# Performance work log

Measured on AMD Instinct MI355X. Metric: run time of the kernel, lower is better.

Reference implementation:

```python
import jax, jax.numpy as jnp
import numpy as np

D_MODEL = 1024
NUM_HEADS = 16
D_HEAD = D_MODEL // NUM_HEADS


def setup_inputs() -> dict:
    key = jax.random.key(0)
    ks = jax.random.split(key, 7)
    B, S = 2, 2048
    scale = 1.0 / np.sqrt(D_MODEL)
    return {
        "x": jax.random.normal(ks[0], (B, S, D_MODEL), dtype=jnp.float32),
        "attn_weights": jnp.zeros((1,), dtype=jnp.float32),  # unused in original forward
        "Wq": jax.random.normal(ks[1], (D_MODEL, D_MODEL), dtype=jnp.float32) * scale,
        "Wk": jax.random.normal(ks[2], (D_MODEL, D_MODEL), dtype=jnp.float32) * scale,
        "Wv": jax.random.normal(ks[3], (D_MODEL, D_MODEL), dtype=jnp.float32) * scale,
        "Wp": jax.random.normal(ks[4], (D_MODEL, D_MODEL), dtype=jnp.float32) * scale,
        "bp": jnp.zeros((D_MODEL,), dtype=jnp.float32),
    }


def reference(x, attn_weights, Wq, Wk, Wv, Wp, bp):
    B, S, D = x.shape
    H, Dh = NUM_HEADS, D_HEAD
    # torch Linear: y = x @ W.T  (weights stored [out, in])
    q = (x @ Wq.T).reshape(B, S, H, Dh).transpose(0, 2, 1, 3)  # [B,H,S,Dh]
    k = (x @ Wk.T).reshape(B, S, H, Dh).transpose(0, 2, 1, 3)
    v = (x @ Wv.T).reshape(B, S, H, Dh).transpose(0, 2, 1, 3)
    # NOTE: original module applies NO 1/sqrt(d) scaling
    scores = jnp.einsum("bhqd,bhkd->bhqk", q, k)
    weights = jax.nn.softmax(scores, axis=-1)  # dropout is inference no-op
    out = jnp.einsum("bhqk,bhkd->bhqd", weights, v)
    out = out.transpose(0, 2, 1, 3).reshape(B, S, D)
    return out @ Wp.T + bp
```

## Files before the change

### kernel.cpp

```cpp
#include <hip/hip_runtime.h>
#include <hip/hip_bf16.h>

#define D_MODEL 1024
#define NUM_HEADS 16
#define D_HEAD 64
#define BATCH 2
#define SEQ 2048
#define TOKENS (BATCH * SEQ)

typedef __attribute__((ext_vector_type(8))) short bf16x8;
typedef __attribute__((ext_vector_type(4))) float f32x4;
typedef __attribute__((ext_vector_type(2))) unsigned int uint2v;

typedef __attribute__((address_space(1))) const unsigned int as1_uint;
typedef __attribute__((address_space(3))) unsigned int as3_uint;

#define LOG2E 1.44269504088896340736f

static __device__ __forceinline__ unsigned short f2bf(float f) {
    unsigned int u = __builtin_bit_cast(unsigned int, f);
    u += 0x7fffu + ((u >> 16) & 1u);
    return (unsigned short)(u >> 16);
}

static __device__ __forceinline__ unsigned int pk2bf(float a, float b) {
    __hip_bfloat162 h = __float22bfloat162_rn(float2{a, b});
    unsigned int u;
    __builtin_memcpy(&u, &h, 4);
    return u;
}

static __device__ __forceinline__ float fast_exp2(float x) {
    return __builtin_amdgcn_exp2f(x);
}

__global__ __launch_bounds__(256) void convert_bf16(
    const float* __restrict__ x,  const float* __restrict__ Wq,
    const float* __restrict__ Wk, const float* __restrict__ Wv,
    const float* __restrict__ Wp,
    unsigned short* __restrict__ xb,  unsigned short* __restrict__ Wqb,
    unsigned short* __restrict__ Wkb, unsigned short* __restrict__ Wvb,
    unsigned short* __restrict__ Wpb)
{
    int v = blockIdx.x * 256 + threadIdx.x;
    const float* s;
    unsigned short* d;
    int off;
    if (v < (1 << 20)) { s = x; d = xb; off = v; }
    else {
        int u = v - (1 << 20);
        int w = u >> 18;
        off = u & ((1 << 18) - 1);
        s = (w == 0) ? Wq : (w == 1) ? Wk : (w == 2) ? Wv : Wp;
        d = (w == 0) ? Wqb : (w == 1) ? Wkb : (w == 2) ? Wvb : Wpb;
    }
    float4 f = ((const float4*)s)[off];
    ushort4 o = { f2bf(f.x), f2bf(f.y), f2bf(f.z), f2bf(f.w) };
    ((ushort4*)d)[off] = o;
}

__global__ __launch_bounds__(512, 4) void qkv_gemm(
    const unsigned short* __restrict__ xb,
    const unsigned short* __restrict__ Wqb, const unsigned short* __restrict__ Wkb,
    const unsigned short* __restrict__ Wvb,
    unsigned short* __restrict__ Q, unsigned short* __restrict__ Kb,
    unsigned short* __restrict__ Vt)
{
    const int m0 = blockIdx.x * 128;
    const int n0 = blockIdx.y * 64;

    __shared__ __attribute__((aligned(16))) unsigned short sm[40960];

    const int t = threadIdx.x;
    const int wave = t >> 6, lane = t & 63;
    const int wm = (wave & 1) * 64, wn = (wave >> 1) * 16;
    const int l15 = lane & 15, quad = lane >> 4;
    const int sw = l15 & 7;

    const unsigned short* Wz[3] = { Wqb, Wkb, Wvb };

    f32x4 acc[3][4];
#pragma unroll
    for (int z = 0; z < 3; z++)
#pragma unroll
        for (int i = 0; i < 4; i++) acc[z][i] = (f32x4)0.f;

    auto stage = [&](int k0, int buf) {
#pragma unroll
        for (int i = 0; i < 2; i++) {
            int fbase = wave * 64 + i * 512;
            int f = fbase + lane;
            int row = f >> 3, cp = f & 7;
            int c = cp ^ (row & 7);
            __builtin_amdgcn_global_load_lds(
                (as1_uint*)&xb[(size_t)(m0 + row) * D_MODEL + k0 + c * 8],
                (as3_uint*)&sm[buf * 20480 + fbase * 8], 16, 0, 0);
        }
        {
            int row = t >> 3, cp = t & 7;
            int c = cp ^ (row & 7);
            int fbase = wave * 64;
#pragma unroll
            for (int z = 0; z < 3; z++)
                __builtin_amdgcn_global_load_lds(
                    (as1_uint*)&Wz[z][(size_t)(n0 + row) * D_MODEL + k0 + c * 8],
                    (as3_uint*)&sm[buf * 20480 + 8192 + z * 4096 + fbase * 8],
                    16, 0, 0);
        }
    };

    stage(0, 0);
    __syncthreads();

    int cur = 0;
    for (int k0 = 0; k0 < D_MODEL; k0 += 64) {
        if (k0 + 64 < D_MODEL) stage(k0 + 64, cur ^ 1);

        const unsigned short* lA = &sm[cur * 20480];
#pragma unroll
        for (int kk = 0; kk < 2; kk++) {
            const int cc = ((kk * 4 + quad) ^ sw) * 8;
            bf16x8 a[4];
#pragma unroll
            for (int mt = 0; mt < 4; mt++)
                a[mt] = *(const bf16x8*)&lA[(wm + mt * 16 + l15) * 64 + cc];
#pragma unroll
            for (int z = 0; z < 3; z++) {
                const unsigned short* lB = &sm[cur * 20480 + 8192 + z * 4096];
                bf16x8 b = *(const bf16x8*)&lB[(wn + l15) * 64 + cc];
#pragma unroll
                for (int mt = 0; mt < 4; mt++)
                    acc[z][mt] = __builtin_amdgcn_mfma_f32_16x16x32_bf16(
                        a[mt], b, acc[z][mt], 0, 0, 0);
            }
        }
        __syncthreads();
        cur ^= 1;
    }

#pragma unroll
    for (int mt = 0; mt < 4; mt++)
#pragma unroll
        for (int r = 0; r < 4; r++) {
            int row = m0 + wm + mt * 16 + quad * 4 + r;
            int col = n0 + wn + l15;
            Q[(size_t)row * D_MODEL + col]  = f2bf(acc[0][mt][r] * LOG2E);
            Kb[(size_t)row * D_MODEL + col] = f2bf(acc[1][mt][r]);
        }
    {
        const int b = m0 >> 11;
        const int srow = (m0 & 2047) + wm + quad * 4;
        const int h = n0 >> 6;
        const int dh = wn + l15;
#pragma unroll
        for (int mt = 0; mt < 4; mt++) {
            ushort4 pk = { f2bf(acc[2][mt][0]), f2bf(acc[2][mt][1]),
                           f2bf(acc[2][mt][2]), f2bf(acc[2][mt][3]) };
            *(ushort4*)&Vt[(size_t)((b * 16 + h) * 64 + dh) * SEQ + srow + mt * 16] = pk;
        }
    }
}

__global__ __launch_bounds__(512, 4) void attn(
    const unsigned short* __restrict__ Q, const unsigned short* __restrict__ K,
    const unsigned short* __restrict__ Vt, unsigned short* __restrict__ O)
{
    const int q0 = blockIdx.y * 128;
    const int bh = blockIdx.x;
    const int b = bh >> 4, h = bh & 15;
    const size_t base = (size_t)b * SEQ * D_MODEL + (size_t)h * D_HEAD;
    const size_t baseV = (size_t)bh * D_HEAD * SEQ;

    __shared__ __attribute__((aligned(16))) char smem[65536];
    unsigned short* lds = (unsigned short*)smem;

    const int t = threadIdx.x;
    const int wave = t >> 6, lane = t & 63;
    const int l15 = lane & 15, quad = lane >> 4;
    const int wq = wave & 3;
    const int sh = wave >> 2;
    const int qw = q0 + wq * 32;
    const int sbase = sh * (SEQ / 2);

    bf16x8 ones;
#pragma unroll
    for (int i = 0; i < 8; i++) ones[i] = (short)0x3F80;

    bf16x8 bq[2][2];
#pragma unroll
    for (int mq = 0; mq < 2; mq++)
#pragma unroll
        for (int kk = 0; kk < 2; kk++)
            bq[mq][kk] = *(const bf16x8*)&Q[base +
                (size_t)(qw + mq * 16 + l15) * D_MODEL + kk * 32 + quad * 8];

    const int tl = t & 255;
    const int sw = l15 & 7;

    auto stage = [&](int soff, int buf) {
#pragma unroll
        for (int i = 0; i < 2; i++) {
            int f = tl + i * 256;
            int row = f >> 3;
            int c = (f & 7) ^ (row & 7);
            __builtin_amdgcn_global_load_lds(
                (as1_uint*)&K[base + (size_t)(sbase + soff + row) * D_MODEL + c * 8],
                (as3_uint*)&lds[buf * 16384 + sh * 4096 + f * 8], 16, 0, 0);
            __builtin_amdgcn_global_load_lds(
                (as1_uint*)&Vt[baseV + (size_t)row * SEQ + sbase + soff + c * 8],
                (as3_uint*)&lds[8192 + buf * 16384 + sh * 4096 + f * 8], 16, 0, 0);
        }
    };

    f32x4 o_acc[2][4];
#pragma unroll
    for (int i = 0; i < 2; i++)
#pragma unroll
        for (int j = 0; j < 4; j++) o_acc[i][j] = (f32x4)0.f;
    f32x4 o_l[2];
#pragma unroll
    for (int i = 0; i < 2; i++) o_l[i] = (f32x4)0.f;

    stage(0, 0);
    __syncthreads();

    int cur = 0;
    for (int s0 = 0; s0 < SEQ / 2; s0 += 64) {
        if (s0 + 64 < SEQ / 2) stage(s0 + 64, cur ^ 1);

        const unsigned short* lK  = lds + cur * 16384 + sh * 4096;
        const unsigned short* lVt = lds + 8192 + cur * 16384 + sh * 4096;

        f32x4 st[4][2];
#pragma unroll
        for (int mt = 0; mt < 4; mt++)
#pragma unroll
            for (int mq = 0; mq < 2; mq++) st[mt][mq] = (f32x4)0.f;
#pragma unroll
        for (int kk = 0; kk < 2; kk++) {
            const int cc = ((kk * 4 + quad) ^ sw) * 8;
#pragma unroll
            for (int mt = 0; mt < 4; mt++) {
                bf16x8 ak = *(const bf16x8*)&lK[(mt * 16 + l15) * 64 + cc];
#pragma unroll
                for (int mq = 0; mq < 2; mq++)
                    st[mt][mq] = __builtin_amdgcn_mfma_f32_16x16x32_bf16(
                        ak, bq[mq][kk], st[mt][mq], 0, 0, 0);
            }
        }

#pragma unroll
        for (int mq = 0; mq < 2; mq++)
#pragma unroll
            for (int mt = 0; mt < 4; mt++)
#pragma unroll
                for (int r = 0; r < 4; r++)
                    st[mt][mq][r] = fast_exp2(st[mt][mq][r]);

        bf16x8 pa[2][2];
#pragma unroll
        for (int mq = 0; mq < 2; mq++)
#pragma unroll
            for (int kk = 0; kk < 2; kk++) {
                unsigned int cw[4];
#pragma unroll
                for (int j = 0; j < 2; j++) {
                    unsigned int w0 = pk2bf(st[2 * kk][mq][2 * j],
                                            st[2 * kk][mq][2 * j + 1]);
                    unsigned int w1 = pk2bf(st[2 * kk + 1][mq][2 * j],
                                            st[2 * kk + 1][mq][2 * j + 1]);
                    uint2v uv = __builtin_amdgcn_permlane32_swap(w0, w1, false, false);
                    uint2v f  = __builtin_amdgcn_permlane16_swap(uv[0], uv[1], false, false);
                    cw[j]     = f[0];
                    cw[2 + j] = f[1];
                }
                union { unsigned int w[4]; bf16x8 v; } uu;
                uu.w[0] = cw[0]; uu.w[1] = cw[1]; uu.w[2] = cw[2]; uu.w[3] = cw[3];
                pa[mq][kk] = uu.v;
            }

#pragma unroll
        for (int kk = 0; kk < 2; kk++) {
            const int cc = ((kk * 4 + quad) ^ sw) * 8;
            bf16x8 bv[4];
#pragma unroll
            for (int nt = 0; nt < 4; nt++)
                bv[nt] = *(const bf16x8*)&lVt[(nt * 16 + l15) * 64 + cc];
#pragma unroll
            for (int mq = 0; mq < 2; mq++) {
#pragma unroll
                for (int nt = 0; nt < 4; nt++)
                    o_acc[mq][nt] = __builtin_amdgcn_mfma_f32_16x16x32_bf16(
                        pa[mq][kk], bv[nt], o_acc[mq][nt], 0, 0, 0);
                o_l[mq] = __builtin_amdgcn_mfma_f32_16x16x32_bf16(
                    pa[mq][kk], ones, o_l[mq], 0, 0, 0);
            }
        }
        __syncthreads();
        cur ^= 1;
    }

    float* sO = (float*)&smem[0];
    float* sL = (float*)&smem[36864];
    if (sh == 1) {
#pragma unroll
        for (int mq = 0; mq < 2; mq++) {
#pragma unroll
            for (int r = 0; r < 4; r++)
                sL[wq * 32 + mq * 16 + quad * 4 + r] = o_l[mq][r];
#pragma unroll
            for (int nt = 0; nt < 4; nt++)
#pragma unroll
                for (int r = 0; r < 4; r++)
                    sO[(wq * 32 + mq * 16 + quad * 4 + r) * 68 + nt * 16 + l15] =
                        o_acc[mq][nt][r];
        }
    }
    __syncthreads();
    if (sh == 0) {
#pragma unroll
        for (int mq = 0; mq < 2; mq++) {
            float inv[4];
#pragma unroll
            for (int r = 0; r < 4; r++)
                inv[r] = 1.f / (o_l[mq][r] + sL[wq * 32 + mq * 16 + quad * 4 + r]);
#pragma unroll
            for (int nt = 0; nt < 4; nt++)
#pragma unroll
                for (int r = 0; r < 4; r++) {
                    int row = qw + mq * 16 + quad * 4 + r;
                    float v = o_acc[mq][nt][r] +
                              sO[(wq * 32 + mq * 16 + quad * 4 + r) * 68 + nt * 16 + l15];
                    O[base + (size_t)row * D_MODEL + nt * 16 + l15] = f2bf(v * inv[r]);
                }
        }
    }
}

__global__ __launch_bounds__(512, 4) void proj_gemm(
    const unsigned short* __restrict__ A, const unsigned short* __restrict__ W,
    const float* __restrict__ bias, float* __restrict__ out)
{
    const int m0 = blockIdx.x * 128;
    const int n0 = blockIdx.y * 64;

    __shared__ __attribute__((aligned(16))) unsigned short sm[24576];

    const int t = threadIdx.x;
    const int wave = t >> 6, lane = t & 63;
    const int wm = (wave & 1) * 64, wn = (wave >> 1) * 16;
    const int l15 = lane & 15, quad = lane >> 4;
    const int sw = l15 & 7;

    f32x4 acc[4];
#pragma unroll
    for (int i = 0; i < 4; i++) acc[i] = (f32x4)0.f;

    auto stage = [&](int k0, int buf) {
#pragma unroll
        for (int i = 0; i < 2; i++) {
            int fbase = wave * 64 + i * 512;
            int f = fbase + lane;
            int row = f >> 3, cp = f & 7;
            int c = cp ^ (row & 7);
            __builtin_amdgcn_global_load_lds(
                (as1_uint*)&A[(size_t)(m0 + row) * D_MODEL + k0 + c * 8],
                (as3_uint*)&sm[buf * 12288 + fbase * 8], 16, 0, 0);
        }
        {
            int row = t >> 3, cp = t & 7;
            int c = cp ^ (row & 7);
            int fbase = wave * 64;
            __builtin_amdgcn_global_load_lds(
                (as1_uint*)&W[(size_t)(n0 + row) * D_MODEL + k0 + c * 8],
                (as3_uint*)&sm[buf * 12288 + 8192 + fbase * 8], 16, 0, 0);
        }
    };

    stage(0, 0);
    __syncthreads();

    int cur = 0;
    for (int k0 = 0; k0 < D_MODEL; k0 += 64) {
        if (k0 + 64 < D_MODEL) stage(k0 + 64, cur ^ 1);

        const unsigned short* lA = &sm[cur * 12288];
        const unsigned short* lB = &sm[cur * 12288 + 8192];
#pragma unroll
        for (int kk = 0; kk < 2; kk++) {
            const int cc = ((kk * 4 + quad) ^ sw) * 8;
            bf16x8 a[4];
#pragma unroll
            for (int mt = 0; mt < 4; mt++)
                a[mt] = *(const bf16x8*)&lA[(wm + mt * 16 + l15) * 64 + cc];
            bf16x8 b = *(const bf16x8*)&lB[(wn + l15) * 64 + cc];
#pragma unroll
            for (int mt = 0; mt < 4; mt++)
                acc[mt] = __builtin_amdgcn_mfma_f32_16x16x32_bf16(
                    a[mt], b, acc[mt], 0, 0, 0);
        }
        __syncthreads();
        cur ^= 1;
    }

    const int col = n0 + wn + l15;
    const float bc = bias[col];
#pragma unroll
    for (int mt = 0; mt < 4; mt++)
#pragma unroll
        for (int r = 0; r < 4; r++) {
            int row = m0 + wm + mt * 16 + quad * 4 + r;
            out[(size_t)row * D_MODEL + col] = acc[mt][r] + bc;
        }
}

extern "C" void kernel_launch(void* const* d_in, const int* in_sizes, int n_in,
                              void* d_out, int out_size, void* d_ws, size_t ws_size,
                              hipStream_t stream)
{
    const float* x  = (const float*)d_in[0];
    const float* Wq = (const float*)d_in[2];
    const float* Wk = (const float*)d_in[3];
    const float* Wv = (const float*)d_in[4];
    const float* Wp = (const float*)d_in[5];
    const float* bp = (const float*)d_in[6];
    float* out = (float*)d_out;

    unsigned short* Q   = (unsigned short*)d_ws;
    unsigned short* K   = Q   + (size_t)TOKENS * D_MODEL;
    unsigned short* Vt  = K   + (size_t)TOKENS * D_MODEL;
    unsigned short* O   = Vt  + (size_t)TOKENS * D_MODEL;
    unsigned short* xb  = O   + (size_t)TOKENS * D_MODEL;
    unsigned short* Wqb = xb  + (size_t)TOKENS * D_MODEL;
    unsigned short* Wkb = Wqb + (size_t)D_MODEL * D_MODEL;
    unsigned short* Wvb = Wkb + (size_t)D_MODEL * D_MODEL;
    unsigned short* Wpb = Wvb + (size_t)D_MODEL * D_MODEL;

    convert_bf16<<<8192, 256, 0, stream>>>(x, Wq, Wk, Wv, Wp,
                                           xb, Wqb, Wkb, Wvb, Wpb);
    qkv_gemm<<<dim3(TOKENS / 128, D_MODEL / 64), 512, 0, stream>>>(
        xb, Wqb, Wkb, Wvb, Q, K, Vt);
    attn<<<dim3(BATCH * NUM_HEADS, SEQ / 128), 512, 0, stream>>>(Q, K, Vt, O);
    proj_gemm<<<dim3(TOKENS / 128, D_MODEL / 64), 512, 0, stream>>>(O, Wpb, bp, out);
}
```

Baseline: 173.5 us.

## Fuse fp32-to-bf16 conversion of x into QKV GEMM loads; raise MFMA priority

The separate conversion pass over x is removed. The QKV GEMM now loads fp32 x through registers, converts it to bf16 and writes it to LDS after the MFMA work of each k-step, so the global load overlaps compute. This drops one full write and re-read of a bf16 copy of x and shrinks the weight-conversion launch. The cost is that each of the 16 column blocks rereads fp32 x at twice the bytes, and extra registers are needed. The attention kernel also raises wave priority around its MFMA sections with s_setprio.

```diff
diff --git a/kernel.cpp b/kernel.cpp
--- a/kernel.cpp
+++ b/kernel.cpp
@@ -34,33 +34,24 @@
     return __builtin_amdgcn_exp2f(x);
 }
 
-__global__ __launch_bounds__(256) void convert_bf16(
-    const float* __restrict__ x,  const float* __restrict__ Wq,
-    const float* __restrict__ Wk, const float* __restrict__ Wv,
-    const float* __restrict__ Wp,
-    unsigned short* __restrict__ xb,  unsigned short* __restrict__ Wqb,
-    unsigned short* __restrict__ Wkb, unsigned short* __restrict__ Wvb,
-    unsigned short* __restrict__ Wpb)
+__global__ __launch_bounds__(256) void convert_w(
+    const float* __restrict__ Wq, const float* __restrict__ Wk,
+    const float* __restrict__ Wv, const float* __restrict__ Wp,
+    unsigned short* __restrict__ Wqb, unsigned short* __restrict__ Wkb,
+    unsigned short* __restrict__ Wvb, unsigned short* __restrict__ Wpb)
 {
     int v = blockIdx.x * 256 + threadIdx.x;
-    const float* s;
-    unsigned short* d;
-    int off;
-    if (v < (1 << 20)) { s = x; d = xb; off = v; }
-    else {
-        int u = v - (1 << 20);
-        int w = u >> 18;
-        off = u & ((1 << 18) - 1);
-        s = (w == 0) ? Wq : (w == 1) ? Wk : (w == 2) ? Wv : Wp;
-        d = (w == 0) ? Wqb : (w == 1) ? Wkb : (w == 2) ? Wvb : Wpb;
-    }
+    int w = v >> 18;
+    int off = v & ((1 << 18) - 1);
+    const float* s = (w == 0) ? Wq : (w == 1) ? Wk : (w == 2) ? Wv : Wp;
+    unsigned short* d = (w == 0) ? Wqb : (w == 1) ? Wkb : (w == 2) ? Wvb : Wpb;
     float4 f = ((const float4*)s)[off];
     ushort4 o = { f2bf(f.x), f2bf(f.y), f2bf(f.z), f2bf(f.w) };
     ((ushort4*)d)[off] = o;
 }
 
 __global__ __launch_bounds__(512, 4) void qkv_gemm(
-    const unsigned short* __restrict__ xb,
+    const float* __restrict__ x,
     const unsigned short* __restrict__ Wqb, const unsigned short* __restrict__ Wkb,
     const unsigned short* __restrict__ Wvb,
     unsigned short* __restrict__ Q, unsigned short* __restrict__ Kb,
@@ -85,36 +76,52 @@
 #pragma unroll
         for (int i = 0; i < 4; i++) acc[z][i] = (f32x4)0.f;
 
-    auto stage = [&](int k0, int buf) {
+    auto stageW = [&](int k0, int buf) {
+        int row = t >> 3, cp = t & 7;
+        int c = cp ^ (row & 7);
+        int fbase = wave * 64;
+#pragma unroll
+        for (int z = 0; z < 3; z++)
+            __builtin_amdgcn_global_load_lds(
+                (as1_uint*)&Wz[z][(size_t)(n0 + row) * D_MODEL + k0 + c * 8],
+                (as3_uint*)&sm[buf * 20480 + 8192 + z * 4096 + fbase * 8],
+                16, 0, 0);
+    };
+
+    float4 ar[2][2];
+    auto loadA = [&](int k0) {
 #pragma unroll
         for (int i = 0; i < 2; i++) {
-            int fbase = wave * 64 + i * 512;
-            int f = fbase + lane;
+            int f = wave * 64 + i * 512 + lane;
             int row = f >> 3, cp = f & 7;
             int c = cp ^ (row & 7);
-            __builtin_amdgcn_global_load_lds(
-                (as1_uint*)&xb[(size_t)(m0 + row) * D_MODEL + k0 + c * 8],
-                (as3_uint*)&sm[buf * 20480 + fbase * 8], 16, 0, 0);
-        }
-        {
-            int row = t >> 3, cp = t & 7;
-            int c = cp ^ (row & 7);
-            int fbase = wave * 64;
-#pragma unroll
-            for (int z = 0; z < 3; z++)
-                __builtin_amdgcn_global_load_lds(
-                    (as1_uint*)&Wz[z][(size_t)(n0 + row) * D_MODEL + k0 + c * 8],
-                    (as3_uint*)&sm[buf * 20480 + 8192 + z * 4096 + fbase * 8],
-                    16, 0, 0);
+            const float4* p = (const float4*)&x[(size_t)(m0 + row) * D_MODEL + k0 + c * 8];
+            ar[i][0] = p[0];
+            ar[i][1] = p[1];
         }
     };
-
-    stage(0, 0);
+    auto writeA = [&](int buf) {
+#pragma unroll
+        for (int i = 0; i < 2; i++) {
+            int f = wave * 64 + i * 512 + lane;
+            union { unsigned short s[8]; uint4 v; } u;
+            u.s[0] = f2bf(ar[i][0].x); u.s[1] = f2bf(ar[i][0].y);
+            u.s[2] = f2bf(ar[i][0].z); u.s[3] = f2bf(ar[i][0].w);
+            u.s[4] = f2bf(ar[i][1].x); u.s[5] = f2bf(ar[i][1].y);
+            u.s[6] = f2bf(ar[i][1].z); u.s[7] = f2bf(ar[i][1].w);
+            *(uint4*)&sm[buf * 20480 + f * 8] = u.v;
+        }
+    };
+
+    loadA(0);
+    stageW(0, 0);
+    writeA(0);
     __syncthreads();
 
     int cur = 0;
     for (int k0 = 0; k0 < D_MODEL; k0 += 64) {
-        if (k0 + 64 < D_MODEL) stage(k0 + 64, cur ^ 1);
+        bool more = (k0 + 64 < D_MODEL);
+        if (more) { stageW(k0 + 64, cur ^ 1); loadA(k0 + 64); }
 
         const unsigned short* lA = &sm[cur * 20480];
 #pragma unroll
@@ -134,6 +141,7 @@
                         a[mt], b, acc[z][mt], 0, 0, 0);
             }
         }
+        if (more) writeA(cur ^ 1);
         __syncthreads();
         cur ^= 1;
     }
@@ -236,6 +244,7 @@
         for (int mt = 0; mt < 4; mt++)
 #pragma unroll
             for (int mq = 0; mq < 2; mq++) st[mt][mq] = (f32x4)0.f;
+        __builtin_amdgcn_s_setprio(1);
 #pragma unroll
         for (int kk = 0; kk < 2; kk++) {
             const int cc = ((kk * 4 + quad) ^ sw) * 8;
@@ -248,6 +257,7 @@
                         ak, bq[mq][kk], st[mt][mq], 0, 0, 0);
             }
         }
+        __builtin_amdgcn_s_setprio(0);
 
 #pragma unroll
         for (int mq = 0; mq < 2; mq++)
@@ -279,6 +289,7 @@
                 pa[mq][kk] = uu.v;
             }
 
+        __builtin_amdgcn_s_setprio(1);
 #pragma unroll
         for (int kk = 0; kk < 2; kk++) {
             const int cc = ((kk * 4 + quad) ^ sw) * 8;
@@ -296,6 +307,7 @@
                     pa[mq][kk], ones, o_l[mq], 0, 0, 0);
             }
         }
+        __builtin_amdgcn_s_setprio(0);
         __syncthreads();
         cur ^= 1;
     }
@@ -430,16 +442,15 @@
     unsigned short* K   = Q   + (size_t)TOKENS * D_MODEL;
     unsigned short* Vt  = K   + (size_t)TOKENS * D_MODEL;
     unsigned short* O   = Vt  + (size_t)TOKENS * D_MODEL;
-    unsigned short* xb  = O   + (size_t)TOKENS * D_MODEL;
-    unsigned short* Wqb = xb  + (size_t)TOKENS * D_MODEL;
+    unsigned short* Wqb = O   + (size_t)TOKENS * D_MODEL;
     unsigned short* Wkb = Wqb + (size_t)D_MODEL * D_MODEL;
     unsigned short* Wvb = Wkb + (size_t)D_MODEL * D_MODEL;
     unsigned short* Wpb = Wvb + (size_t)D_MODEL * D_MODEL;
 
-    convert_bf16<<<8192, 256, 0, stream>>>(x, Wq, Wk, Wv, Wp,
-                                           xb, Wqb, Wkb, Wvb, Wpb);
+    convert_w<<<4096, 256, 0, stream>>>(Wq, Wk, Wv, Wp,
+                                        Wqb, Wkb, Wvb, Wpb);
     qkv_gemm<<<dim3(TOKENS / 128, D_MODEL / 64), 512, 0, stream>>>(
-        xb, Wqb, Wkb, Wvb, Q, K, Vt);
+        x, Wqb, Wkb, Wvb, Q, K, Vt);
     attn<<<dim3(BATCH * NUM_HEADS, SEQ / 128), 512, 0, stream>>>(Q, K, Vt, O);
     proj_gemm<<<dim3(TOKENS / 128, D_MODEL / 64), 512, 0, stream>>>(O, Wpb, bp, out);
 }
```

New measurement: 172.8 us. No clear change (-0.4%).
